# Optimization experiments

Hardware: AMD Instinct MI355X
Metric: run time of the kernel (lower is better)

## Reference

```python
import jax, jax.numpy as jnp
import numpy as np

N_NODES = 50000
N_EDGES = 800000
D_IN = 128
D_OUT = 128
NEG_SLOPE = 0.2


def setup_inputs() -> dict:
    key = jax.random.key(0)
    ks = jax.random.split(key, 6)
    stdv = 1.0 / np.sqrt(D_OUT)
    X = jax.random.normal(ks[0], (N_NODES, D_IN), dtype=jnp.float32)
    W = jax.random.uniform(ks[1], (D_IN, D_OUT), dtype=jnp.float32, minval=-stdv, maxval=stdv)
    W_r = jax.random.uniform(ks[2], (D_IN, D_OUT), dtype=jnp.float32, minval=-stdv, maxval=stdv)
    W_l = jax.random.uniform(ks[3], (D_IN, D_OUT), dtype=jnp.float32, minval=-stdv, maxval=stdv)
    src = jax.random.randint(ks[4], (N_EDGES,), 0, N_NODES, dtype=jnp.int32)
    dst = jax.random.randint(ks[5], (N_EDGES,), 0, N_NODES, dtype=jnp.int32)
    return {"X": X, "W": W, "W_r": W_r, "W_l": W_l, "src": src, "dst": dst}


def reference(X, W, W_r, W_l, src, dst):
    # Dense transforms (comb/agg feature paths)
    comb = X @ W            # [N, D_out]
    h_r = X @ W_r           # [N, D_out]
    h_l = X @ W_l           # [N, D_out]
    # SDDMM: per-edge score e_ij = dot(h_l[i], h_r[j]) at nonzeros of A
    e = jnp.sum(h_l[src] * h_r[dst], axis=-1)          # [E]
    e = jax.nn.leaky_relu(e, negative_slope=NEG_SLOPE)  # LeakyReLU(0.2) on edge values
    # SpMM aggregation: agg[i] = sum_{j in N(i)} e_ij * comb[j]
    msgs = e[:, None] * comb[dst]                       # [E, D_out]
    agg = jax.ops.segment_sum(msgs, src, num_segments=N_NODES)  # [N, D_out]
    return agg
```

## Files before the change

### kernel.cpp

```cpp
#include <hip/hip_runtime.h>
#include <hip/hip_bf16.h>

#define N_NODES 50000
#define N_EDGES 800000
#define D 128
#define NEG_SLOPE 0.2f
#define APAD 136

#define FB 196
#define BCAP 8192
#define CHUNK 2048
#define BIN_NBLK ((N_EDGES + CHUNK - 1) / CHUNK)
#define GROWS 64
#define GGRID ((N_NODES + GROWS - 1) / GROWS)
#define GEMM_LDS (D * APAD * 2 + GROWS * APAD * 2)

#define SPMM_NODES 16
#define SPMM_GRID (N_NODES / SPMM_NODES)
#define SPMM_LDS ((D * APAD + SPMM_NODES * APAD) * 2)

typedef __attribute__((ext_vector_type(8))) short bf16x8;
typedef __attribute__((ext_vector_type(4))) float f32x4;

__device__ inline unsigned short f2bf(float f) {
    union { float f; unsigned u; } v; v.f = f;
    const unsigned r = v.u + 0x7FFF + ((v.u >> 16) & 1);
    return (unsigned short)(r >> 16);
}
__device__ inline unsigned fbits(float f) { union { float f; unsigned u; } v; v.f = f; return v.u; }
__device__ inline float ffrom(unsigned u) { union { unsigned u; float f; } v; v.u = u; return v.f; }

__device__ inline void unpack8(const float4 raw, float* o) {
    const unsigned w0 = fbits(raw.x), w1 = fbits(raw.y), w2 = fbits(raw.z), w3 = fbits(raw.w);
    o[0] = ffrom(w0 << 16); o[1] = ffrom(w0 & 0xffff0000u);
    o[2] = ffrom(w1 << 16); o[3] = ffrom(w1 & 0xffff0000u);
    o[4] = ffrom(w2 << 16); o[5] = ffrom(w2 & 0xffff0000u);
    o[6] = ffrom(w3 << 16); o[7] = ffrom(w3 & 0xffff0000u);
}

__device__ __forceinline__ float rsum16(float t) {
    union { float f; int i; } u, s;
    u.f = t;
    s.i = __builtin_amdgcn_update_dpp(0, u.i, 0x128, 0xF, 0xF, true); u.f += s.f;
    s.i = __builtin_amdgcn_update_dpp(0, u.i, 0x124, 0xF, 0xF, true); u.f += s.f;
    s.i = __builtin_amdgcn_update_dpp(0, u.i, 0x4E,  0xF, 0xF, true); u.f += s.f;
    s.i = __builtin_amdgcn_update_dpp(0, u.i, 0x39,  0xF, 0xF, true); u.f += s.f;
    return u.f;
}

__device__ __forceinline__ int scan256_incl_fast(int* wsum, int t, int v) {
    const int lane = t & 63;
    int x = v;
#pragma unroll
    for (int off = 1; off < 64; off <<= 1) {
        const int u = __shfl_up(x, off, 64);
        if (lane >= off) x += u;
    }
    if (lane == 63) wsum[t >> 6] = x;
    __syncthreads();
    int base = 0;
#pragma unroll
    for (int wv = 0; wv < 3; ++wv)
        base += (wv < (t >> 6)) ? wsum[wv] : 0;
    return x + base;
}

__device__ __forceinline__ int scan_incl_512(int* wsum, int t, int v) {
    const int lane = t & 63;
    int x = v;
#pragma unroll
    for (int off = 1; off < 64; off <<= 1) {
        const int u = __shfl_up(x, off, 64);
        if (lane >= off) x += u;
    }
    if (lane == 63) wsum[t >> 6] = x;
    __syncthreads();
    int base = 0;
#pragma unroll
    for (int wv = 0; wv < 7; ++wv)
        base += (wv < (t >> 6)) ? wsum[wv] : 0;
    return x + base;
}

__device__ __forceinline__ void stage_B_lds(unsigned short* Bs, const ushort* __restrict__ BT) {
    const int tid = threadIdx.x;
#pragma unroll
    for (int i = 0; i < 8; ++i) {
        const int idx = tid + i * 256;
        const int row = idx >> 4;
        const int c8 = (idx & 15) << 3;
        const float4 v = ((const float4*)BT)[idx];
        *(float4*)&Bs[row * APAD + c8] = v;
    }
}

template <bool OUT_F32>
__device__ __forceinline__ void mfma_from_lds(const unsigned short* Bs,
                                              const unsigned short* As,
                                              int rb, float* __restrict__ Cf,
                                              ushort* __restrict__ Cb, int nrows) {
    const int tid = threadIdx.x;
    const int w = tid >> 6, lane = tid & 63, m = lane & 15, kq = lane >> 4;
    f32x4 acc[8] = {};
    const unsigned short* Arow = &As[(w * 16 + m) * APAD + kq * 8];
#pragma unroll
    for (int kc = 0; kc < 4; ++kc) {
        const bf16x8 af = *(const bf16x8*)(Arow + kc * 32);
#pragma unroll
        for (int t2 = 0; t2 < 8; ++t2) {
            const bf16x8 bf = *(const bf16x8*)&Bs[(t2 * 16 + m) * APAD + kc * 32 + kq * 8];
            acc[t2] = __builtin_amdgcn_mfma_f32_16x16x32_bf16(af, bf, acc[t2], 0, 0, 0);
        }
    }
    const int orow0 = rb + w * 16 + kq * 4;
#pragma unroll
    for (int t2 = 0; t2 < 8; ++t2) {
#pragma unroll
        for (int r = 0; r < 4; ++r) {
            const int row = orow0 + r;
            if (row < nrows) {
                const size_t o = (size_t)row * D + t2 * 16 + m;
                if (OUT_F32) Cf[o] = acc[t2][r];
                else         Cb[o] = f2bf(acc[t2][r]);
            }
        }
    }
}

__global__ __launch_bounds__(256) void prep_kernel(const float* __restrict__ W_l,
                                                   const float* __restrict__ W_r,
                                                   const float* __restrict__ W,
                                                   ushort* __restrict__ MbT,
                                                   ushort* __restrict__ WbT,
                                                   int* __restrict__ bucket_fill) {
    if (blockIdx.x == 0) bucket_fill[threadIdx.x] = 0;
    const int a = blockIdx.x * 2 + (threadIdx.x >> 7);
    const int b2 = threadIdx.x & 127;
    float acc = 0.f;
#pragma unroll
    for (int c = 0; c < D; c += 4) {
        const float4 wl = *(const float4*)(W_l + a * D + c);
        const float4 wr = *(const float4*)(W_r + b2 * D + c);
        acc += wl.x * wr.x + wl.y * wr.y + wl.z * wr.z + wl.w * wr.w;
    }
    MbT[b2 * D + a] = f2bf(acc);
    WbT[b2 * D + a] = f2bf(W[a * D + b2]);
}

__global__ __launch_bounds__(256) void k1_kernel(const int* __restrict__ src,
                                                 const int* __restrict__ dst,
                                                 int* __restrict__ bucket_fill,
                                                 int2* __restrict__ binned,
                                                 const ushort* __restrict__ MbT,
                                                 const float4* __restrict__ Xf4,
                                                 ushort* __restrict__ Xb,
                                                 ushort* __restrict__ hMb) {
    __shared__ __align__(16) char smem[GEMM_LDS];
    const int bx = blockIdx.x;
    const int t = threadIdx.x;

    if (bx < BIN_NBLK) {
        int*  hist     = (int*)smem;
        int*  bstart   = hist + 256;
        int*  reserveS = bstart + 256;
        int*  fillL    = reserveS + 256;
        int2* pairs    = (int2*)(fillL + 256);
        int*  targ     = (int*)(pairs + CHUNK);
        const int e0 = bx * CHUNK;

        hist[t] = 0;
        __syncthreads();

        int s[8], d[8], b[8];
#pragma unroll
        for (int i = 0; i < 8; ++i) {
            const int e = e0 + i * 256 + t;
            if (e < N_EDGES) {
                s[i] = src[e]; d[i] = dst[e]; b[i] = s[i] >> 8;
                atomicAdd(&hist[b[i]], 1);
            } else b[i] = -1;
        }
        __syncthreads();
        const int hv = hist[t];
        const int incl = scan256_incl_fast(bstart, t, hv);
        const int mystart = incl - hv;
        reserveS[t] = hv ? atomicAdd(&bucket_fill[t], hv) : 0;
        __syncthreads();
        bstart[t] = mystart;
        fillL[t] = mystart;
        __syncthreads();
#pragma unroll
        for (int i = 0; i < 8; ++i) {
            if (b[i] >= 0) {
                const int p = atomicAdd(&fillL[b[i]], 1);
                pairs[p] = make_int2(s[i], d[i]);
                const int pos = reserveS[b[i]] + (p - bstart[b[i]]);
                targ[p] = (pos < BCAP) ? (b[i] * BCAP + pos) : -1;
            }
        }
        __syncthreads();
        const int nval = min(CHUNK, N_EDGES - e0);
        for (int j = t; j < nval; j += 256)
            if (targ[j] >= 0) binned[targ[j]] = pairs[j];
    } else {
        unsigned short* Bs = (unsigned short*)smem;
        unsigned short* As = Bs + D * APAD;
        const int rb = (bx - BIN_NBLK) * GROWS;

        stage_B_lds(Bs, MbT);
#pragma unroll
        for (int i = 0; i < 4; ++i) {
            const int f2 = t + i * 256;
            const int row = f2 >> 4;
            const int c8 = (f2 & 15) << 3;
            ushort4 lo = {0, 0, 0, 0}, hi = {0, 0, 0, 0};
            if (rb + row < N_NODES) {
                const float4 a = Xf4[(size_t)(rb + row) * 32 + (c8 >> 2)];
                const float4 b = Xf4[(size_t)(rb + row) * 32 + (c8 >> 2) + 1];
                lo.x = f2bf(a.x); lo.y = f2bf(a.y); lo.z = f2bf(a.z); lo.w = f2bf(a.w);
                hi.x = f2bf(b.x); hi.y = f2bf(b.y); hi.z = f2bf(b.z); hi.w = f2bf(b.w);
                ushort* gp = Xb + (size_t)(rb + row) * D + c8;
                *(ushort4*)gp = lo;
                *(ushort4*)(gp + 4) = hi;
            }
            *(ushort4*)&As[row * APAD + c8] = lo;
            *(ushort4*)&As[row * APAD + c8 + 4] = hi;
        }
        __syncthreads();
        mfma_from_lds<false>(Bs, As, rb, nullptr, hMb, N_NODES);
    }
}

__global__ __launch_bounds__(512) void fine_kernel(const int2* __restrict__ binned,
                                                   const int* __restrict__ bucket_fill,
                                                   int* __restrict__ offsets,
                                                   int* __restrict__ sorted_dst) {
    __shared__ int cntS[256];
    __shared__ int nh[256];
    __shared__ int fill[256];
    __shared__ int wsum[8];
    __shared__ int dstbuf[BCAP];
    const int b = blockIdx.x;
    const int t = threadIdx.x;

    int cv = 0;
    if (t < 256) cv = (t < FB) ? bucket_fill[t] : 0;
    const int incl = scan_incl_512(wsum, t, cv);
    if (t < 256) cntS[t] = incl;
    __syncthreads();
    const int base = (b == 0) ? 0 : cntS[b - 1];
    int cnt = cntS[b] - base;
    if (cnt > BCAP) cnt = BCAP;

    if (t < 256) nh[t] = 0;
    __syncthreads();
    const int2* bb = binned + (size_t)b * BCAP;
    for (int e = t; e < cnt; e += 512) atomicAdd(&nh[bb[e].x & 255], 1);
    __syncthreads();
    const int v = (t < 256) ? nh[t] : 0;
    const int incl2 = scan_incl_512(wsum, t, v);
    if (t < 256) {
        const int mystart = incl2 - v;
        const int node = b * 256 + t;
        if (node < N_NODES) offsets[node] = base + mystart;
        fill[t] = mystart;
    }
    __syncthreads();
    for (int e = t; e < cnt; e += 512) {
        const int2 sd = bb[e];
        const int p = atomicAdd(&fill[sd.x & 255], 1);
        dstbuf[p] = sd.y;
    }
    __syncthreads();
    for (int j = t; j < cnt; j += 512)
        sorted_dst[base + j] = dstbuf[j];
}

__global__ __launch_bounds__(1024, 8) void spmm_fused_kernel(const ushort* __restrict__ hMb,
                                                             const ushort* __restrict__ Xb,
                                                             const int* __restrict__ offsets,
                                                             const int* __restrict__ sorted_dst,
                                                             const ushort* __restrict__ WbT,
                                                             float* __restrict__ agg) {
    __shared__ __align__(16) char smem[SPMM_LDS];
    unsigned short* Ws = (unsigned short*)smem;
    unsigned short* As = Ws + D * APAD;
    const int tid = threadIdx.x;

#pragma unroll
    for (int i = 0; i < 2; ++i) {
        const int idx = tid + i * 1024;
        const int row = idx >> 4;
        const int c8 = (idx & 15) << 3;
        const float4 v = ((const float4*)WbT)[idx];
        *(float4*)&Ws[row * APAD + c8] = v;
    }

    const int wave = tid >> 6;
    const int lane = tid & 63;
    const int node = blockIdx.x * SPMM_NODES + wave;
    const int q = lane >> 4;
    const int ql = lane & 15;

    float hm[8];
    unpack8(*(const float4*)(hMb + (size_t)node * D + ql * 8), hm);

    const int start = offsets[node];
    const int end = (node == N_NODES - 1) ? N_EDGES : offsets[node + 1];

    float acc[8] = {0.f, 0.f, 0.f, 0.f, 0.f, 0.f, 0.f, 0.f};

    int idx = start + q;
    while (idx + 12 < end) {
        const int d0 = sorted_dst[idx];
        const int d1 = sorted_dst[idx + 4];
        const int d2 = sorted_dst[idx + 8];
        const int d3 = sorted_dst[idx + 12];
        const float4 r0 = *(const float4*)(Xb + (size_t)d0 * D + ql * 8);
        const float4 r1 = *(const float4*)(Xb + (size_t)d1 * D + ql * 8);
        const float4 r2 = *(const float4*)(Xb + (size_t)d2 * D + ql * 8);
        const float4 r3 = *(const float4*)(Xb + (size_t)d3 * D + ql * 8);
        float t0 = 0.f, t1 = 0.f, t2 = 0.f, t3 = 0.f;
        {
            float x[8];
            unpack8(r0, x);
#pragma unroll
            for (int j = 0; j < 8; ++j) t0 = fmaf(hm[j], x[j], t0);
            unpack8(r1, x);
#pragma unroll
            for (int j = 0; j < 8; ++j) t1 = fmaf(hm[j], x[j], t1);
            unpack8(r2, x);
#pragma unroll
            for (int j = 0; j < 8; ++j) t2 = fmaf(hm[j], x[j], t2);
            unpack8(r3, x);
#pragma unroll
            for (int j = 0; j < 8; ++j) t3 = fmaf(hm[j], x[j], t3);
        }
        t0 = rsum16(t0);
        t1 = rsum16(t1);
        t2 = rsum16(t2);
        t3 = rsum16(t3);
        const float e0 = t0 > 0.f ? t0 : NEG_SLOPE * t0;
        const float e1 = t1 > 0.f ? t1 : NEG_SLOPE * t1;
        const float e2 = t2 > 0.f ? t2 : NEG_SLOPE * t2;
        const float e3 = t3 > 0.f ? t3 : NEG_SLOPE * t3;
        {
            float x[8];
            unpack8(r0, x);
#pragma unroll
            for (int j = 0; j < 8; ++j) acc[j] = fmaf(e0, x[j], acc[j]);
            unpack8(r1, x);
#pragma unroll
            for (int j = 0; j < 8; ++j) acc[j] = fmaf(e1, x[j], acc[j]);
            unpack8(r2, x);
#pragma unroll
            for (int j = 0; j < 8; ++j) acc[j] = fmaf(e2, x[j], acc[j]);
            unpack8(r3, x);
#pragma unroll
            for (int j = 0; j < 8; ++j) acc[j] = fmaf(e3, x[j], acc[j]);
        }
        idx += 16;
    }
    if (idx < end) {
        const int i1 = idx + 4, i2 = idx + 8;
        const bool v1 = i1 < end, v2 = i2 < end;
        const int d0 = sorted_dst[idx];
        const int d1 = sorted_dst[v1 ? i1 : idx];
        const int d2 = sorted_dst[v2 ? i2 : idx];
        const float4 r0 = *(const float4*)(Xb + (size_t)d0 * D + ql * 8);
        const float4 r1 = *(const float4*)(Xb + (size_t)d1 * D + ql * 8);
        const float4 r2 = *(const float4*)(Xb + (size_t)d2 * D + ql * 8);
        float t0 = 0.f, t1 = 0.f, t2 = 0.f;
        {
            float x[8];
            unpack8(r0, x);
#pragma unroll
            for (int j = 0; j < 8; ++j) t0 = fmaf(hm[j], x[j], t0);
            unpack8(r1, x);
#pragma unroll
            for (int j = 0; j < 8; ++j) t1 = fmaf(hm[j], x[j], t1);
            unpack8(r2, x);
#pragma unroll
            for (int j = 0; j < 8; ++j) t2 = fmaf(hm[j], x[j], t2);
        }
        t0 = rsum16(t0);
        t1 = rsum16(t1);
        t2 = rsum16(t2);
        float e0 = t0 > 0.f ? t0 : NEG_SLOPE * t0;
        float e1 = t1 > 0.f ? t1 : NEG_SLOPE * t1;
        float e2 = t2 > 0.f ? t2 : NEG_SLOPE * t2;
        e1 = v1 ? e1 : 0.f;
        e2 = v2 ? e2 : 0.f;
        {
            float x[8];
            unpack8(r0, x);
#pragma unroll
            for (int j = 0; j < 8; ++j) acc[j] = fmaf(e0, x[j], acc[j]);
            unpack8(r1, x);
#pragma unroll
            for (int j = 0; j < 8; ++j) acc[j] = fmaf(e1, x[j], acc[j]);
            unpack8(r2, x);
#pragma unroll
            for (int j = 0; j < 8; ++j) acc[j] = fmaf(e2, x[j], acc[j]);
        }
    }

#pragma unroll
    for (int j = 0; j < 8; ++j) {
        acc[j] += __shfl_xor(acc[j], 16);
        acc[j] += __shfl_xor(acc[j], 32);
    }
    if (q == 0) {
        ushort4 o0, o1;
        o0.x = f2bf(acc[0]); o0.y = f2bf(acc[1]); o0.z = f2bf(acc[2]); o0.w = f2bf(acc[3]);
        o1.x = f2bf(acc[4]); o1.y = f2bf(acc[5]); o1.z = f2bf(acc[6]); o1.w = f2bf(acc[7]);
        *(ushort4*)&As[wave * APAD + ql * 8] = o0;
        *(ushort4*)&As[wave * APAD + ql * 8 + 4] = o1;
    }
    __syncthreads();

    if (wave < 4) {
        const int m = lane & 15, kq = lane >> 4;
        f32x4 oacc[2] = {};
        const unsigned short* Arow = &As[m * APAD + kq * 8];
#pragma unroll
        for (int kc = 0; kc < 4; ++kc) {
            const bf16x8 af = *(const bf16x8*)(Arow + kc * 32);
#pragma unroll
            for (int tt = 0; tt < 2; ++tt) {
                const int t2 = wave * 2 + tt;
                const bf16x8 bf = *(const bf16x8*)&Ws[(t2 * 16 + m) * APAD + kc * 32 + kq * 8];
                oacc[tt] = __builtin_amdgcn_mfma_f32_16x16x32_bf16(af, bf, oacc[tt], 0, 0, 0);
            }
        }
        const int rbase = blockIdx.x * SPMM_NODES + kq * 4;
#pragma unroll
        for (int tt = 0; tt < 2; ++tt) {
            const int t2 = wave * 2 + tt;
#pragma unroll
            for (int r = 0; r < 4; ++r) {
                agg[(size_t)(rbase + r) * D + t2 * 16 + m] = oacc[tt][r];
            }
        }
    }
}

extern "C" void kernel_launch(void* const* d_in, const int* in_sizes, int n_in,
                              void* d_out, int out_size, void* d_ws, size_t ws_size,
                              hipStream_t stream) {
    const float* X   = (const float*)d_in[0];
    const float* W   = (const float*)d_in[1];
    const float* W_r = (const float*)d_in[2];
    const float* W_l = (const float*)d_in[3];
    const int* src   = (const int*)d_in[4];
    const int* dst   = (const int*)d_in[5];
    float* agg = (float*)d_out;

    ushort* Xb          = (ushort*)d_ws;
    ushort* hMb         = Xb + (size_t)N_NODES * D;
    ushort* aggXb       = hMb + (size_t)N_NODES * D;
    ushort* MbT         = aggXb + (size_t)N_NODES * D;
    ushort* WbT         = MbT + D * D;
    int*    offsets     = (int*)(WbT + D * D);
    int*    sorted_dst  = offsets + N_NODES;
    int*    bucket_fill = sorted_dst + N_EDGES;
    int2*   binned      = (int2*)(bucket_fill + 256);

    prep_kernel<<<64, 256, 0, stream>>>(W_l, W_r, W, MbT, WbT, bucket_fill);

    k1_kernel<<<BIN_NBLK + GGRID, 256, 0, stream>>>(
        src, dst, bucket_fill, binned, MbT, (const float4*)X, Xb, hMb);

    fine_kernel<<<FB, 512, 0, stream>>>(binned, bucket_fill, offsets, sorted_dst);

    spmm_fused_kernel<<<SPMM_GRID, 1024, 0, stream>>>(
        hMb, Xb, offsets, sorted_dst, WbT, agg);
}
```

Baseline: 156.3 us.

## Replace two-level bucket sort with global counting sort via atomics

Replaces the coarse binning into fixed-capacity buckets followed by a per-bucket LDS sort with a plain counting sort. Per-node degrees are counted with global atomics, two small kernels compute exclusive offsets, and a scatter kernel places dst indices using global atomic fill counters. This removes the BCAP overflow truncation and the int2 intermediate buffer, but adds two kernel launches and many contended global atomics. Edge order within a node becomes nondeterministic.

```diff
diff --git a/kernel.cpp b/kernel.cpp
--- a/kernel.cpp
+++ b/kernel.cpp
@@ -8,7 +8,7 @@
 #define APAD 136
 
 #define FB 196
-#define BCAP 8192
+#define NC_PAD (FB * 256)
 #define CHUNK 2048
 #define BIN_NBLK ((N_EDGES + CHUNK - 1) / CHUNK)
 #define GROWS 64
@@ -61,23 +61,6 @@
     int base = 0;
 #pragma unroll
     for (int wv = 0; wv < 3; ++wv)
-        base += (wv < (t >> 6)) ? wsum[wv] : 0;
-    return x + base;
-}
-
-__device__ __forceinline__ int scan_incl_512(int* wsum, int t, int v) {
-    const int lane = t & 63;
-    int x = v;
-#pragma unroll
-    for (int off = 1; off < 64; off <<= 1) {
-        const int u = __shfl_up(x, off, 64);
-        if (lane >= off) x += u;
-    }
-    if (lane == 63) wsum[t >> 6] = x;
-    __syncthreads();
-    int base = 0;
-#pragma unroll
-    for (int wv = 0; wv < 7; ++wv)
         base += (wv < (t >> 6)) ? wsum[wv] : 0;
     return x + base;
 }
@@ -132,8 +115,9 @@
                                                    const float* __restrict__ W,
                                                    ushort* __restrict__ MbT,
                                                    ushort* __restrict__ WbT,
-                                                   int* __restrict__ bucket_fill) {
-    if (blockIdx.x == 0) bucket_fill[threadIdx.x] = 0;
+                                                   int* __restrict__ node_cnt) {
+    for (int k = blockIdx.x * 256 + threadIdx.x; k < NC_PAD; k += 64 * 256)
+        node_cnt[k] = 0;
     const int a = blockIdx.x * 2 + (threadIdx.x >> 7);
     const int b2 = threadIdx.x & 127;
     float acc = 0.f;
@@ -148,9 +132,7 @@
 }
 
 __global__ __launch_bounds__(256) void k1_kernel(const int* __restrict__ src,
-                                                 const int* __restrict__ dst,
-                                                 int* __restrict__ bucket_fill,
-                                                 int2* __restrict__ binned,
+                                                 int* __restrict__ node_cnt,
                                                  const ushort* __restrict__ MbT,
                                                  const float4* __restrict__ Xf4,
                                                  ushort* __restrict__ Xb,
@@ -160,48 +142,12 @@
     const int t = threadIdx.x;
 
     if (bx < BIN_NBLK) {
-        int*  hist     = (int*)smem;
-        int*  bstart   = hist + 256;
-        int*  reserveS = bstart + 256;
-        int*  fillL    = reserveS + 256;
-        int2* pairs    = (int2*)(fillL + 256);
-        int*  targ     = (int*)(pairs + CHUNK);
         const int e0 = bx * CHUNK;
-
-        hist[t] = 0;
-        __syncthreads();
-
-        int s[8], d[8], b[8];
 #pragma unroll
         for (int i = 0; i < 8; ++i) {
             const int e = e0 + i * 256 + t;
-            if (e < N_EDGES) {
-                s[i] = src[e]; d[i] = dst[e]; b[i] = s[i] >> 8;
-                atomicAdd(&hist[b[i]], 1);
-            } else b[i] = -1;
-        }
-        __syncthreads();
-        const int hv = hist[t];
-        const int incl = scan256_incl_fast(bstart, t, hv);
-        const int mystart = incl - hv;
-        reserveS[t] = hv ? atomicAdd(&bucket_fill[t], hv) : 0;
-        __syncthreads();
-        bstart[t] = mystart;
-        fillL[t] = mystart;
-        __syncthreads();
-#pragma unroll
-        for (int i = 0; i < 8; ++i) {
-            if (b[i] >= 0) {
-                const int p = atomicAdd(&fillL[b[i]], 1);
-                pairs[p] = make_int2(s[i], d[i]);
-                const int pos = reserveS[b[i]] + (p - bstart[b[i]]);
-                targ[p] = (pos < BCAP) ? (b[i] * BCAP + pos) : -1;
-            }
-        }
-        __syncthreads();
-        const int nval = min(CHUNK, N_EDGES - e0);
-        for (int j = t; j < nval; j += 256)
-            if (targ[j] >= 0) binned[targ[j]] = pairs[j];
+            if (e < N_EDGES) atomicAdd(&node_cnt[src[e]], 1);
+        }
     } else {
         unsigned short* Bs = (unsigned short*)smem;
         unsigned short* As = Bs + D * APAD;
@@ -231,49 +177,52 @@
     }
 }
 
-__global__ __launch_bounds__(512) void fine_kernel(const int2* __restrict__ binned,
-                                                   const int* __restrict__ bucket_fill,
-                                                   int* __restrict__ offsets,
-                                                   int* __restrict__ sorted_dst) {
-    __shared__ int cntS[256];
-    __shared__ int nh[256];
-    __shared__ int fill[256];
-    __shared__ int wsum[8];
-    __shared__ int dstbuf[BCAP];
-    const int b = blockIdx.x;
+__global__ __launch_bounds__(256) void scanA_kernel(const int* __restrict__ node_cnt,
+                                                    int* __restrict__ bucket_total) {
     const int t = threadIdx.x;
-
-    int cv = 0;
-    if (t < 256) cv = (t < FB) ? bucket_fill[t] : 0;
-    const int incl = scan_incl_512(wsum, t, cv);
-    if (t < 256) cntS[t] = incl;
+    int v = node_cnt[blockIdx.x * 256 + t];
+#pragma unroll
+    for (int off = 1; off < 64; off <<= 1) v += __shfl_xor(v, off, 64);
+    __shared__ int ws[4];
+    if ((t & 63) == 0) ws[t >> 6] = v;
     __syncthreads();
-    const int base = (b == 0) ? 0 : cntS[b - 1];
-    int cnt = cntS[b] - base;
-    if (cnt > BCAP) cnt = BCAP;
-
-    if (t < 256) nh[t] = 0;
+    if (t == 0) bucket_total[blockIdx.x] = ws[0] + ws[1] + ws[2] + ws[3];
+}
+
+__global__ __launch_bounds__(256) void scanB_kernel(const int* __restrict__ node_cnt,
+                                                    const int* __restrict__ bucket_total,
+                                                    int* __restrict__ offsets,
+                                                    int* __restrict__ fillg) {
+    __shared__ int wsum[4];
+    __shared__ int sbt[256];
+    const int b = blockIdx.x, t = threadIdx.x;
+    const int bt = (t < FB) ? bucket_total[t] : 0;
+    const int binc = scan256_incl_fast(wsum, t, bt);
+    sbt[t] = binc;
     __syncthreads();
-    const int2* bb = binned + (size_t)b * BCAP;
-    for (int e = t; e < cnt; e += 512) atomicAdd(&nh[bb[e].x & 255], 1);
-    __syncthreads();
-    const int v = (t < 256) ? nh[t] : 0;
-    const int incl2 = scan_incl_512(wsum, t, v);
-    if (t < 256) {
-        const int mystart = incl2 - v;
-        const int node = b * 256 + t;
-        if (node < N_NODES) offsets[node] = base + mystart;
-        fill[t] = mystart;
-    }
-    __syncthreads();
-    for (int e = t; e < cnt; e += 512) {
-        const int2 sd = bb[e];
-        const int p = atomicAdd(&fill[sd.x & 255], 1);
-        dstbuf[p] = sd.y;
-    }
-    __syncthreads();
-    for (int j = t; j < cnt; j += 512)
-        sorted_dst[base + j] = dstbuf[j];
+    const int base = (b == 0) ? 0 : sbt[b - 1];
+    const int v = node_cnt[b * 256 + t];
+    const int incl = scan256_incl_fast(wsum, t, v);
+    const int off = base + incl - v;
+    offsets[b * 256 + t] = off;
+    fillg[b * 256 + t] = off;
+}
+
+__global__ __launch_bounds__(256) void scatter_kernel(const int* __restrict__ src,
+                                                      const int* __restrict__ dst,
+                                                      int* __restrict__ fillg,
+                                                      int* __restrict__ sorted_dst) {
+    const int e0 = blockIdx.x * CHUNK;
+    const int t = threadIdx.x;
+#pragma unroll
+    for (int i = 0; i < 8; ++i) {
+        const int e = e0 + i * 256 + t;
+        if (e < N_EDGES) {
+            const int s = src[e];
+            const int p = atomicAdd(&fillg[s], 1);
+            sorted_dst[p] = dst[e];
+        }
+    }
 }
 
 __global__ __launch_bounds__(1024, 8) void spmm_fused_kernel(const ushort* __restrict__ hMb,
@@ -456,22 +405,26 @@
     const int* dst   = (const int*)d_in[5];
     float* agg = (float*)d_out;
 
-    ushort* Xb          = (ushort*)d_ws;
-    ushort* hMb         = Xb + (size_t)N_NODES * D;
-    ushort* aggXb       = hMb + (size_t)N_NODES * D;
-    ushort* MbT         = aggXb + (size_t)N_NODES * D;
-    ushort* WbT         = MbT + D * D;
-    int*    offsets     = (int*)(WbT + D * D);
-    int*    sorted_dst  = offsets + N_NODES;
-    int*    bucket_fill = sorted_dst + N_EDGES;
-    int2*   binned      = (int2*)(bucket_fill + 256);
-
-    prep_kernel<<<64, 256, 0, stream>>>(W_l, W_r, W, MbT, WbT, bucket_fill);
+    ushort* Xb           = (ushort*)d_ws;
+    ushort* hMb          = Xb + (size_t)N_NODES * D;
+    ushort* MbT          = hMb + (size_t)N_NODES * D;
+    ushort* WbT          = MbT + D * D;
+    int*    offsets      = (int*)(WbT + D * D);
+    int*    fillg        = offsets + NC_PAD;
+    int*    node_cnt     = fillg + NC_PAD;
+    int*    bucket_total = node_cnt + NC_PAD;
+    int*    sorted_dst   = bucket_total + 256;
+
+    prep_kernel<<<64, 256, 0, stream>>>(W_l, W_r, W, MbT, WbT, node_cnt);
 
     k1_kernel<<<BIN_NBLK + GGRID, 256, 0, stream>>>(
-        src, dst, bucket_fill, binned, MbT, (const float4*)X, Xb, hMb);
-
-    fine_kernel<<<FB, 512, 0, stream>>>(binned, bucket_fill, offsets, sorted_dst);
+        src, node_cnt, MbT, (const float4*)X, Xb, hMb);
+
+    scanA_kernel<<<FB, 256, 0, stream>>>(node_cnt, bucket_total);
+
+    scanB_kernel<<<FB, 256, 0, stream>>>(node_cnt, bucket_total, offsets, fillg);
+
+    scatter_kernel<<<BIN_NBLK, 256, 0, stream>>>(src, dst, fillg, sorted_dst);
 
     spmm_fused_kernel<<<SPMM_GRID, 1024, 0, stream>>>(
         hMb, Xb, offsets, sorted_dst, WbT, agg);
```

Result: slower. 230.4 us (+47.4%).

## Split each node's edge list across two waves with LDS partial-sum reduction

Applied to the files above, without the earlier changes.

The fused SpMM kernel now assigns two waves per node (8 nodes per block instead of 16), each handling interleaved halves of the edge list, and combines their partial accumulators through a new float LDS buffer before the bf16 MFMA projection. This doubles the grid size and halves per-wave serial edge work, aiming to improve latency hiding and load balance on skewed degree distributions. The cost is an extra LDS round trip and sync, less in-flight loads per wave (2 edges per iteration instead of 4), wasted MFMA rows (padded with zeros), and re-staging W into LDS twice as many times. Also removes an unused workspace buffer.

```diff
diff --git a/kernel.cpp b/kernel.cpp
--- a/kernel.cpp
+++ b/kernel.cpp
@@ -15,9 +15,9 @@
 #define GGRID ((N_NODES + GROWS - 1) / GROWS)
 #define GEMM_LDS (D * APAD * 2 + GROWS * APAD * 2)
 
-#define SPMM_NODES 16
+#define SPMM_NODES 8
 #define SPMM_GRID (N_NODES / SPMM_NODES)
-#define SPMM_LDS ((D * APAD + SPMM_NODES * APAD) * 2)
+#define SPMM_LDS (D * APAD * 2 + 16 * APAD * 2 + 16 * 132 * 4)
 
 typedef __attribute__((ext_vector_type(8))) short bf16x8;
 typedef __attribute__((ext_vector_type(4))) float f32x4;
@@ -285,6 +285,7 @@
     __shared__ __align__(16) char smem[SPMM_LDS];
     unsigned short* Ws = (unsigned short*)smem;
     unsigned short* As = Ws + D * APAD;
+    float*          Pf = (float*)(As + 16 * APAD);
     const int tid = threadIdx.x;
 
 #pragma unroll
@@ -295,10 +296,13 @@
         const float4 v = ((const float4*)WbT)[idx];
         *(float4*)&Ws[row * APAD + c8] = v;
     }
+    if (tid < 272) ((ushort4*)(As + 8 * APAD))[tid] = make_ushort4(0, 0, 0, 0);
 
     const int wave = tid >> 6;
     const int lane = tid & 63;
-    const int node = blockIdx.x * SPMM_NODES + wave;
+    const int h = wave & 1;
+    const int nl = wave >> 1;
+    const int node = blockIdx.x * SPMM_NODES + nl;
     const int q = lane >> 4;
     const int ql = lane & 15;
 
@@ -310,17 +314,13 @@
 
     float acc[8] = {0.f, 0.f, 0.f, 0.f, 0.f, 0.f, 0.f, 0.f};
 
-    int idx = start + q;
-    while (idx + 12 < end) {
+    int idx = start + h * 4 + q;
+    while (idx + 8 < end) {
         const int d0 = sorted_dst[idx];
-        const int d1 = sorted_dst[idx + 4];
-        const int d2 = sorted_dst[idx + 8];
-        const int d3 = sorted_dst[idx + 12];
+        const int d1 = sorted_dst[idx + 8];
         const float4 r0 = *(const float4*)(Xb + (size_t)d0 * D + ql * 8);
         const float4 r1 = *(const float4*)(Xb + (size_t)d1 * D + ql * 8);
-        const float4 r2 = *(const float4*)(Xb + (size_t)d2 * D + ql * 8);
-        const float4 r3 = *(const float4*)(Xb + (size_t)d3 * D + ql * 8);
-        float t0 = 0.f, t1 = 0.f, t2 = 0.f, t3 = 0.f;
+        float t0 = 0.f, t1 = 0.f;
         {
             float x[8];
             unpack8(r0, x);
@@ -329,21 +329,11 @@
             unpack8(r1, x);
 #pragma unroll
             for (int j = 0; j < 8; ++j) t1 = fmaf(hm[j], x[j], t1);
-            unpack8(r2, x);
-#pragma unroll
-            for (int j = 0; j < 8; ++j) t2 = fmaf(hm[j], x[j], t2);
-            unpack8(r3, x);
-#pragma unroll
-            for (int j = 0; j < 8; ++j) t3 = fmaf(hm[j], x[j], t3);
         }
         t0 = rsum16(t0);
         t1 = rsum16(t1);
-        t2 = rsum16(t2);
-        t3 = rsum16(t3);
         const float e0 = t0 > 0.f ? t0 : NEG_SLOPE * t0;
         const float e1 = t1 > 0.f ? t1 : NEG_SLOPE * t1;
-        const float e2 = t2 > 0.f ? t2 : NEG_SLOPE * t2;
-        const float e3 = t3 > 0.f ? t3 : NEG_SLOPE * t3;
         {
             float x[8];
             unpack8(r0, x);
@@ -352,56 +342,26 @@
             unpack8(r1, x);
 #pragma unroll
             for (int j = 0; j < 8; ++j) acc[j] = fmaf(e1, x[j], acc[j]);
-            unpack8(r2, x);
-#pragma unroll
-            for (int j = 0; j < 8; ++j) acc[j] = fmaf(e2, x[j], acc[j]);
-            unpack8(r3, x);
-#pragma unroll
-            for (int j = 0; j < 8; ++j) acc[j] = fmaf(e3, x[j], acc[j]);
         }
         idx += 16;
     }
     if (idx < end) {
-        const int i1 = idx + 4, i2 = idx + 8;
-        const bool v1 = i1 < end, v2 = i2 < end;
         const int d0 = sorted_dst[idx];
-        const int d1 = sorted_dst[v1 ? i1 : idx];
-        const int d2 = sorted_dst[v2 ? i2 : idx];
         const float4 r0 = *(const float4*)(Xb + (size_t)d0 * D + ql * 8);
-        const float4 r1 = *(const float4*)(Xb + (size_t)d1 * D + ql * 8);
-        const float4 r2 = *(const float4*)(Xb + (size_t)d2 * D + ql * 8);
-        float t0 = 0.f, t1 = 0.f, t2 = 0.f;
+        float t0 = 0.f;
         {
             float x[8];
             unpack8(r0, x);
 #pragma unroll
             for (int j = 0; j < 8; ++j) t0 = fmaf(hm[j], x[j], t0);
-            unpack8(r1, x);
-#pragma unroll
-            for (int j = 0; j < 8; ++j) t1 = fmaf(hm[j], x[j], t1);
-            unpack8(r2, x);
-#pragma unroll
-            for (int j = 0; j < 8; ++j) t2 = fmaf(hm[j], x[j], t2);
         }
         t0 = rsum16(t0);
-        t1 = rsum16(t1);
-        t2 = rsum16(t2);
-        float e0 = t0 > 0.f ? t0 : NEG_SLOPE * t0;
-        float e1 = t1 > 0.f ? t1 : NEG_SLOPE * t1;
-        float e2 = t2 > 0.f ? t2 : NEG_SLOPE * t2;
-        e1 = v1 ? e1 : 0.f;
-        e2 = v2 ? e2 : 0.f;
+        const float e0 = t0 > 0.f ? t0 : NEG_SLOPE * t0;
         {
             float x[8];
             unpack8(r0, x);
 #pragma unroll
             for (int j = 0; j < 8; ++j) acc[j] = fmaf(e0, x[j], acc[j]);
-            unpack8(r1, x);
-#pragma unroll
-            for (int j = 0; j < 8; ++j) acc[j] = fmaf(e1, x[j], acc[j]);
-            unpack8(r2, x);
-#pragma unroll
-            for (int j = 0; j < 8; ++j) acc[j] = fmaf(e2, x[j], acc[j]);
         }
     }
 
@@ -411,11 +371,22 @@
         acc[j] += __shfl_xor(acc[j], 32);
     }
     if (q == 0) {
+        float* p = Pf + (h * 8 + nl) * 132 + ql * 8;
+#pragma unroll
+        for (int j = 0; j < 8; ++j) p[j] = acc[j];
+    }
+    __syncthreads();
+
+    if (h == 0 && q == 0) {
+        const float* p0 = Pf + nl * 132 + ql * 8;
+        const float* p1 = Pf + (8 + nl) * 132 + ql * 8;
         ushort4 o0, o1;
-        o0.x = f2bf(acc[0]); o0.y = f2bf(acc[1]); o0.z = f2bf(acc[2]); o0.w = f2bf(acc[3]);
-        o1.x = f2bf(acc[4]); o1.y = f2bf(acc[5]); o1.z = f2bf(acc[6]); o1.w = f2bf(acc[7]);
-        *(ushort4*)&As[wave * APAD + ql * 8] = o0;
-        *(ushort4*)&As[wave * APAD + ql * 8 + 4] = o1;
+        o0.x = f2bf(p0[0] + p1[0]); o0.y = f2bf(p0[1] + p1[1]);
+        o0.z = f2bf(p0[2] + p1[2]); o0.w = f2bf(p0[3] + p1[3]);
+        o1.x = f2bf(p0[4] + p1[4]); o1.y = f2bf(p0[5] + p1[5]);
+        o1.z = f2bf(p0[6] + p1[6]); o1.w = f2bf(p0[7] + p1[7]);
+        *(ushort4*)&As[nl * APAD + ql * 8] = o0;
+        *(ushort4*)&As[nl * APAD + ql * 8 + 4] = o1;
     }
     __syncthreads();
 
@@ -433,13 +404,15 @@
                 oacc[tt] = __builtin_amdgcn_mfma_f32_16x16x32_bf16(af, bf, oacc[tt], 0, 0, 0);
             }
         }
-        const int rbase = blockIdx.x * SPMM_NODES + kq * 4;
-#pragma unroll
-        for (int tt = 0; tt < 2; ++tt) {
-            const int t2 = wave * 2 + tt;
-#pragma unroll
-            for (int r = 0; r < 4; ++r) {
-                agg[(size_t)(rbase + r) * D + t2 * 16 + m] = oacc[tt][r];
+        if (kq < 2) {
+            const int rbase = blockIdx.x * SPMM_NODES + kq * 4;
+#pragma unroll
+            for (int tt = 0; tt < 2; ++tt) {
+                const int t2 = wave * 2 + tt;
+#pragma unroll
+                for (int r = 0; r < 4; ++r) {
+                    agg[(size_t)(rbase + r) * D + t2 * 16 + m] = oacc[tt][r];
+                }
             }
         }
     }
@@ -458,8 +431,7 @@
 
     ushort* Xb          = (ushort*)d_ws;
     ushort* hMb         = Xb + (size_t)N_NODES * D;
-    ushort* aggXb       = hMb + (size_t)N_NODES * D;
-    ushort* MbT         = aggXb + (size_t)N_NODES * D;
+    ushort* MbT         = hMb + (size_t)N_NODES * D;
     ushort* WbT         = MbT + D * D;
     int*    offsets     = (int*)(WbT + D * D);
     int*    sorted_dst  = offsets + N_NODES;
```

After: 167.7 us. 1.07x slower.
